# Kernel tuning notes

Measured on AMD Instinct MI355X. Metric: run time of the kernel, lower is better.

Reference implementation:

```python
import jax, jax.numpy as jnp
import numpy as np

B, S, T = 64, 49, 32
ENC, HID, EMB, VOCAB = 512, 512, 512, 32000
ATT = HID  # attention_dim = hidden_size in __init__


def setup_inputs() -> dict:
    key = jax.random.key(0)
    ks = jax.random.split(key, 20)
    def lin(k, out_d, in_d):
        s = 1.0 / np.sqrt(in_d)
        kw, kb = jax.random.split(k)
        return (jax.random.uniform(kw, (out_d, in_d), jnp.float32, -s, s),
                jax.random.uniform(kb, (out_d,), jnp.float32, -s, s))
    W_ih, b_ih = lin(ks[0], 3 * HID, EMB + ENC)
    W_hh, b_hh = lin(ks[1], 3 * HID, HID)
    W_out, b_out = lin(ks[2], VOCAB, HID)
    W_init, b_init = lin(ks[3], HID, ENC)
    W_beta, b_beta = lin(ks[4], ENC, HID)
    W_ea, b_ea = lin(ks[5], ATT, ENC)
    W_da, b_da = lin(ks[6], ATT, HID)
    W_fa, b_fa = lin(ks[7], 1, ATT)
    emb = jax.random.normal(ks[8], (VOCAB, EMB), jnp.float32)
    feats = jax.random.normal(ks[9], (B, S, ENC), jnp.float32)
    seq = jax.random.randint(ks[10], (B, T), 0, VOCAB)
    length = jax.random.randint(ks[11], (B,), 1, T + 1).at[0].set(T)
    return dict(feats=feats, seq=seq, length=length, emb=emb,
                W_ih=W_ih, b_ih=b_ih, W_hh=W_hh, b_hh=b_hh,
                W_out=W_out, b_out=b_out, W_init=W_init, b_init=b_init,
                W_beta=W_beta, b_beta=b_beta, W_ea=W_ea, b_ea=b_ea,
                W_da=W_da, b_da=b_da, W_fa=W_fa, b_fa=b_fa)


def _forward(feats, seq, length, emb, W_ih, b_ih, W_hh, b_hh, W_out, b_out,
             W_init, b_init, W_beta, b_beta, W_ea, b_ea, W_da, b_da, W_fa, b_fa):
    Tlen = seq.shape[1]
    embed_seq = emb[seq]                      # [B, T, EMB]
    embed_seq = jnp.swapaxes(embed_seq, 0, 1)  # [T, B, EMB]
    # active[t, b] = (length[b] > t); equivalent to torch's sorted shrinking batch
    active = (jnp.arange(Tlen)[:, None] < length[None, :])  # [T, B] bool
    h0 = jnp.mean(feats, axis=1) @ W_init.T + b_init         # [B, HID]
    scope0 = jnp.ones(feats.shape[:2], feats.dtype)          # [B, S]
    att1 = feats @ W_ea.T + b_ea                              # [B, S, ATT], hoisted

    def gru_cell(x, h):
        gi = x @ W_ih.T + b_ih
        gh = h @ W_hh.T + b_hh
        ir, iz, inn = jnp.split(gi, 3, axis=1)
        hr, hz, hn = jnp.split(gh, 3, axis=1)
        r = jax.nn.sigmoid(ir + hr)
        z = jax.nn.sigmoid(iz + hz)
        n = jnp.tanh(inn + r * hn)
        return (1.0 - z) * n + z * h

    def step(carry, xs):
        h, scope = carry
        embed_t, act = xs                     # [B, EMB], [B] bool
        actf = act[:, None].astype(h.dtype)
        att2 = h @ W_da.T + b_da              # [B, ATT]
        att = (jax.nn.relu(att1 + att2[:, None, :]) @ W_fa.T).squeeze(-1) + b_fa  # [B, S]
        alpha = jax.nn.softmax(att, axis=1)
        alpha_tilde = scope * alpha
        scope = jnp.where(act[:, None], scope * (1.0 - alpha), scope)
        awe = jnp.einsum('bse,bs->be', feats, alpha)          # [B, ENC]
        gate = jax.nn.sigmoid(h @ W_beta.T + b_beta)
        x = jnp.concatenate([embed_t, gate * awe], axis=1)
        h_new = gru_cell(x, h)
        h = jnp.where(act[:, None], h_new, h)
        preds = h_new @ W_out.T + b_out
        out_t = preds * actf
        alpha_out = alpha_tilde * actf
        return (h, scope), (out_t, alpha_out)

    (_, _), (output, alphas) = jax.lax.scan(step, (h0, scope0), (embed_seq, active))
    output = jnp.swapaxes(output, 0, 1)   # [B, T, VOCAB]
    alphas = jnp.swapaxes(alphas, 0, 1)   # [B, T, S]
    return output, alphas


def reference(feats, seq, length, emb, W_ih, b_ih, W_hh, b_hh, W_out, b_out,
              W_init, b_init, W_beta, b_beta, W_ea, b_ea, W_da, b_da, W_fa, b_fa):
    return _forward(feats, seq, length, emb, W_ih, b_ih, W_hh, b_hh, W_out, b_out,
                    W_init, b_init, W_beta, b_beta, W_ea, b_ea, W_da, b_da, W_fa, b_fa)
```

## Files before the change

### kernel.cpp

```cpp
#include <hip/hip_runtime.h>
#include <cstdint>
#include <cstddef>

#define B_   64
#define S_   49
#define T_   32
#define D_   512
#define V_   32000
#define G3   1536
#define NBLK 64

typedef float v4f   __attribute__((ext_vector_type(4)));
typedef int   i32x4 __attribute__((ext_vector_type(4)));
typedef _Float16 f16;
typedef _Float16 f16x8 __attribute__((ext_vector_type(8)));
typedef _Float16 f16x4 __attribute__((ext_vector_type(4)));

__device__ __forceinline__ float sigm(float x) { return 1.f / (1.f + __expf(-x)); }

__device__ __forceinline__ uint64_t ld_a64(const void* p) {
  return __hip_atomic_load((const uint64_t*)p, __ATOMIC_RELAXED, __HIP_MEMORY_SCOPE_AGENT);
}
__device__ __forceinline__ void st_a64(void* p, uint64_t v) {
  __hip_atomic_store((uint64_t*)p, v, __ATOMIC_RELAXED, __HIP_MEMORY_SCOPE_AGENT);
}
__device__ __forceinline__ uint32_t ld_a32(const void* p) {
  return __hip_atomic_load((const uint32_t*)p, __ATOMIC_RELAXED, __HIP_MEMORY_SCOPE_AGENT);
}
__device__ __forceinline__ void st_a32(void* p, uint32_t v) {
  __hip_atomic_store((uint32_t*)p, v, __ATOMIC_RELAXED, __HIP_MEMORY_SCOPE_AGENT);
}

__global__ __launch_bounds__(256) void k_cvt16(const float* __restrict__ in,
                                               f16* __restrict__ out) {
  int i = (blockIdx.x * 256 + threadIdx.x) * 8;
  float4 a = *(const float4*)(in + i);
  float4 b = *(const float4*)(in + i + 4);
  f16x8 o;
  o[0] = (f16)a.x; o[1] = (f16)a.y; o[2] = (f16)a.z; o[3] = (f16)a.w;
  o[4] = (f16)b.x; o[5] = (f16)b.y; o[6] = (f16)b.z; o[7] = (f16)b.w;
  *(f16x8*)(out + i) = o;
}

__global__ __launch_bounds__(128) void k_embed(const float* __restrict__ emb,
    const int* __restrict__ seq, const int* __restrict__ length,
    f16* __restrict__ xemb16, float* __restrict__ actmask) {
  int m = blockIdx.x;
  int t = m >> 6, b = m & 63;
  int idx = seq[b * T_ + t];
  float4 v = ((const float4*)(emb + (size_t)idx * D_))[threadIdx.x];
  f16x4 o;
  o[0] = (f16)v.x; o[1] = (f16)v.y; o[2] = (f16)v.z; o[3] = (f16)v.w;
  *(f16x4*)(xemb16 + (size_t)m * D_ + threadIdx.x * 4) = o;
  if (threadIdx.x == 0) actmask[b * T_ + t] = (t < length[b]) ? 1.f : 0.f;
}

__global__ __launch_bounds__(256) void k_hmean(const float* __restrict__ feats,
    float* __restrict__ hmean) {
  int b = blockIdx.x, tid = threadIdx.x;
  for (int e = tid; e < D_; e += 256) {
    float s = 0.f;
    for (int si = 0; si < S_; ++si) s += feats[((size_t)b * S_ + si) * D_ + e];
    hmean[b * D_ + e] = s * (1.f / 49.f);
  }
}

__global__ __launch_bounds__(256) void k_gemm_f32(
    float* __restrict__ C, const float* __restrict__ X, const float* __restrict__ W,
    const float* __restrict__ bias, int N, int K, int ldw) {
  __shared__ __align__(16) float XsT[32][68];
  __shared__ __align__(16) float WsT[32][68];
  const int nbase = blockIdx.x * 64, mbase = blockIdx.y * 64;
  const int tid = threadIdx.x;
  const int lr = tid >> 2;
  const int lk = (tid & 3) * 8;
  const int ty = tid >> 4, tx = tid & 15;
  float acc[4][4] = {};
  for (int k0 = 0; k0 < K; k0 += 32) {
    {
      const float* xs = X + (size_t)(mbase + lr) * K + k0 + lk;
      const float* wsrc = W + (size_t)(nbase + lr) * ldw + k0 + lk;
      float4 x0 = *(const float4*)xs, x1 = *(const float4*)(xs + 4);
      float4 w0 = *(const float4*)wsrc, w1 = *(const float4*)(wsrc + 4);
      XsT[lk + 0][lr] = x0.x; XsT[lk + 1][lr] = x0.y; XsT[lk + 2][lr] = x0.z; XsT[lk + 3][lr] = x0.w;
      XsT[lk + 4][lr] = x1.x; XsT[lk + 5][lr] = x1.y; XsT[lk + 6][lr] = x1.z; XsT[lk + 7][lr] = x1.w;
      WsT[lk + 0][lr] = w0.x; WsT[lk + 1][lr] = w0.y; WsT[lk + 2][lr] = w0.z; WsT[lk + 3][lr] = w0.w;
      WsT[lk + 4][lr] = w1.x; WsT[lk + 5][lr] = w1.y; WsT[lk + 6][lr] = w1.z; WsT[lk + 7][lr] = w1.w;
    }
    __syncthreads();
    #pragma unroll
    for (int kk = 0; kk < 32; ++kk) {
      float4 a4 = *(const float4*)&XsT[kk][ty * 4];
      float4 w4 = *(const float4*)&WsT[kk][tx * 4];
      float av[4] = {a4.x, a4.y, a4.z, a4.w};
      float wv[4] = {w4.x, w4.y, w4.z, w4.w};
      #pragma unroll
      for (int i = 0; i < 4; ++i)
        #pragma unroll
        for (int j = 0; j < 4; ++j)
          acc[i][j] = fmaf(av[i], wv[j], acc[i][j]);
    }
    __syncthreads();
  }
  #pragma unroll
  for (int i = 0; i < 4; ++i) {
    int m = mbase + ty * 4 + i;
    int n = nbase + tx * 4;
    float4 o;
    o.x = acc[i][0] + bias[n + 0];
    o.y = acc[i][1] + bias[n + 1];
    o.z = acc[i][2] + bias[n + 2];
    o.w = acc[i][3] + bias[n + 3];
    *(float4*)&C[(size_t)m * N + n] = o;
  }
}

#define GEMM16_CORE                                                            \
  __shared__ __align__(16) f16 As[128 * 32];                                   \
  __shared__ __align__(16) f16 Bs[128 * 32];                                   \
  const int tid = threadIdx.x;                                                 \
  const int l = tid & 63, w = tid >> 6;                                        \
  const int wr = w >> 1, wc = w & 1;                                           \
  const int lm = l & 15;                                                       \
  const int kc = l >> 4;                                                       \
  const int rchunk = (kc ^ ((lm >> 1) & 3)) * 8;                               \
  v4f acc[4][4];                                                               \
  _Pragma("unroll")                                                            \
  for (int mi = 0; mi < 4; ++mi)                                               \
    _Pragma("unroll")                                                          \
    for (int ni = 0; ni < 4; ++ni)                                             \
      acc[mi][ni] = (v4f){0.f, 0.f, 0.f, 0.f};                                 \
  i32x4 ra[2], rb[2];                                                          \
  auto LD = [&](int k0) {                                                      \
    _Pragma("unroll")                                                          \
    for (int i = 0; i < 2; ++i) {                                              \
      int ch = i * 256 + tid;                                                  \
      int row = ch >> 2, cq = ch & 3;                                          \
      ra[i] = *(const i32x4*)&A[(size_t)(mb + row) * 512 + k0 + cq * 8];       \
      rb[i] = *(const i32x4*)&Bw[(size_t)(nb + row) * 512 + k0 + cq * 8];      \
    }                                                                          \
  };                                                                           \
  LD(0);                                                                       \
  for (int k0 = 0; k0 < 512; k0 += 32) {                                       \
    _Pragma("unroll")                                                          \
    for (int i = 0; i < 2; ++i) {                                              \
      int ch = i * 256 + tid;                                                  \
      int row = ch >> 2, cq = ch & 3;                                          \
      int sc = (cq ^ ((row >> 1) & 3)) * 8;                                    \
      *(i32x4*)&As[row * 32 + sc] = ra[i];                                     \
      *(i32x4*)&Bs[row * 32 + sc] = rb[i];                                     \
    }                                                                          \
    __syncthreads();                                                           \
    if (k0 < 480) LD(k0 + 32);                                                 \
    f16x8 af[4], bf[4];                                                        \
    _Pragma("unroll")                                                          \
    for (int mi = 0; mi < 4; ++mi)                                             \
      af[mi] = *(const f16x8*)&As[(wr * 64 + mi * 16 + lm) * 32 + rchunk];     \
    _Pragma("unroll")                                                          \
    for (int ni = 0; ni < 4; ++ni)                                             \
      bf[ni] = *(const f16x8*)&Bs[(wc * 64 + ni * 16 + lm) * 32 + rchunk];     \
    _Pragma("unroll")                                                          \
    for (int mi = 0; mi < 4; ++mi)                                             \
      _Pragma("unroll")                                                        \
      for (int ni = 0; ni < 4; ++ni)                                           \
        acc[mi][ni] = __builtin_amdgcn_mfma_f32_16x16x32_f16(af[mi], bf[ni], acc[mi][ni], 0, 0, 0); \
    __syncthreads();                                                           \
  }

__global__ __launch_bounds__(256) void k_gemm16f(
    const f16* __restrict__ A, const f16* __restrict__ Bw,
    const float* __restrict__ bias, f16* __restrict__ out) {
  const int nb = blockIdx.x * 128, mb = blockIdx.y * 128;
  GEMM16_CORE
  #pragma unroll
  for (int ni = 0; ni < 4; ++ni) {
    int n = nb + wc * 64 + ni * 16 + lm;
    float bo = bias[n];
    #pragma unroll
    for (int mi = 0; mi < 4; ++mi) {
      int m0 = mb + wr * 64 + mi * 16 + (l >> 4) * 4;
      #pragma unroll
      for (int r = 0; r < 4; ++r) {
        int m = m0 + r;
        if (m < B_ * S_) out[(size_t)m * 512 + n] = (f16)(acc[mi][ni][r] + bo);
      }
    }
  }
}

__global__ __launch_bounds__(256) void k_gemm16g(
    const f16* __restrict__ A, const f16* __restrict__ Bw,
    const float* __restrict__ bias, float* __restrict__ out) {
  const int nb = blockIdx.x * 128, mb = blockIdx.y * 128;
  GEMM16_CORE
  #pragma unroll
  for (int ni = 0; ni < 4; ++ni) {
    int n = nb + wc * 64 + ni * 16 + lm;
    float bo = bias[n];
    int gate = n >> 9, rem = n & 511;
    int Kb = rem >> 3, jl = rem & 7;
    #pragma unroll
    for (int mi = 0; mi < 4; ++mi) {
      int m0 = mb + wr * 64 + mi * 16 + (l >> 4) * 4;
      int t = m0 >> 6, b0q = m0 & 63;
      float* dst = out + (((size_t)t * 64 + Kb) * 32 + gate * 8 + jl) * 64 + b0q;
      #pragma unroll
      for (int r = 0; r < 4; ++r)
        dst[r] = acc[mi][ni][r] + bo;
    }
  }
}

__global__ __launch_bounds__(256) void k_packW(
    const float* __restrict__ Wda, const float* __restrict__ Wbe,
    const float* __restrict__ Whh, const float* __restrict__ Wih,
    f16* __restrict__ Wp1, f16* __restrict__ Wp2, f16* __restrict__ Wp3) {
  int K = blockIdx.x, tid = threadIdx.x;
  for (int idx = tid; idx < 40 * 512; idx += 256) {
    int r = idx >> 9, e = idx & 511;
    float v;
    if (r < 8)       v = Wda[(size_t)(8 * K + r) * D_ + e];
    else if (r < 16) v = Wbe[(size_t)(8 * K + r - 8) * D_ + e];
    else if (r < 24) v = Whh[(size_t)(8 * K + r - 16) * D_ + e];
    else if (r < 32) v = Whh[(size_t)(512 + 8 * K + r - 24) * D_ + e];
    else             v = Whh[(size_t)(1024 + 8 * K + r - 32) * D_ + e];
    Wp1[(size_t)K * 20480 + idx] = (f16)v;
  }
  for (int idx = tid; idx < 24 * 512; idx += 256) {
    int r = idx >> 9, e = idx & 511;
    int g = r >> 3, jj = r & 7;
    float v = Wih[(size_t)(g * 512 + 8 * K + jj) * 1024 + 512 + e];
    Wp2[(size_t)K * 12288 + idx] = (f16)v;
  }
  for (int idx = tid; idx < 24 * 512; idx += 256) {
    int rl = idx >> 9, e = idx & 511;
    int r = K * 24 + rl;
    Wp3[(size_t)r * 512 + e] = (f16)Wih[(size_t)r * 1024 + e];
  }
}

__global__ __launch_bounds__(256) void k_packF(
    const float* __restrict__ feats, const float* __restrict__ h0,
    f16* __restrict__ feats16, f16* __restrict__ h16) {
  const int NF = B_ * S_ * D_;
  for (size_t i = blockIdx.x * 256 + threadIdx.x; i < NF + B_ * D_;
       i += (size_t)gridDim.x * 256) {
    if (i < NF) feats16[i] = (f16)feats[i];
    else        h16[i - NF] = (f16)h0[i - NF];
  }
}

__device__ __forceinline__ void wait_flags64(const int* __restrict__ flags,
                                             int target, int tid) {
  if (tid < 64) {
    while (!__all((int)ld_a32(flags + tid * 16) >= target)) {}
  }
  __syncthreads();
}

__device__ __forceinline__ void set_flag(int* slot, int val, int tid) {
  __syncthreads();
  if (tid == 0) st_a32(slot, (uint32_t)val);
}

__device__ __forceinline__ void stage_fast(const f16* __restrict__ src,
                                           uint4* __restrict__ hs, int tid) {
  const i32x4* s = (const i32x4*)src;
  i32x4 v[16];
  #pragma unroll
  for (int i = 0; i < 16; ++i) {
    asm volatile("global_load_dwordx4 %0, %1, off sc0 sc1"
                 : "=v"(v[i]) : "v"(s + i * 256 + tid));
  }
  asm volatile("s_waitcnt vmcnt(0)" ::: "memory");
  __builtin_amdgcn_sched_barrier(0);
  #pragma unroll
  for (int i = 0; i < 16; ++i) {
    int g = i * 256 + tid;
    int b = g >> 6, c = g & 63;
    *(i32x4*)&hs[b * 64 + (c ^ (b & 7))] = v[i];
  }
}

__global__ __launch_bounds__(256, 1) void k_recur(
    const f16* __restrict__ Wp1, const f16* __restrict__ Wp2,
    const f16* __restrict__ att116, const f16* __restrict__ feats16,
    const float* __restrict__ gi_pack,
    const float* __restrict__ b_da, const float* __restrict__ b_beta,
    const float* __restrict__ b_hh,
    const float* __restrict__ W_fa, const float* __restrict__ b_fa,
    const int* __restrict__ length,
    f16* __restrict__ h16, f16* __restrict__ xg16,
    float* __restrict__ att2g,
    float* __restrict__ alphas, f16* __restrict__ Hbuf,
    int* __restrict__ flags) {
  __shared__ __align__(16) uint4 lds_all[8704];
  __shared__ float gh_lds[24 * 72];
  __shared__ float gix_lds[24 * 72];
  __shared__ float att2_s[512];
  __shared__ float gate_s[512];
  __shared__ float att_s[64];
  __shared__ float alpha_s[64];
  uint4* hs = lds_all;
  uint4* W1 = lds_all + 4096;
  uint4* W2 = lds_all + 6656;
  float* attp = (float*)(lds_all + 8192);

  const int K = blockIdx.x, tid = threadIdx.x;
  const int w = tid >> 6, l = tid & 63;
  const int lm = l & 15, c4 = l >> 4;
  const int bq = tid & 63, jg = tid >> 6;
  const int jj0 = 2 * jg, jj1 = 2 * jg + 1;
  int* flagA = flags;
  int* flagB = flags + 1024;
  int* flagC = flags + 2048;

  {
    const uint4* s1 = (const uint4*)(Wp1 + (size_t)K * 20480);
    const uint4* s2 = (const uint4*)(Wp2 + (size_t)K * 12288);
    #pragma unroll
    for (int i = 0; i < 10; ++i) {
      int g = i * 256 + tid;
      int s = g >> 6, c = g & 63;
      W1[s * 64 + (c ^ (s & 7))] = s1[g];
    }
    #pragma unroll
    for (int i = 0; i < 6; ++i) {
      int g = i * 256 + tid;
      int s = g >> 6, c = g & 63;
      W2[s * 64 + (c ^ (s & 7))] = s2[g];
    }
  }
  const int lenB = length[K];
  const float bfa0 = b_fa[0];
  const int lb = length[bq];
  const float bhr0 = b_hh[8 * K + jj0],        bhr1 = b_hh[8 * K + jj1];
  const float bhz0 = b_hh[512 + 8 * K + jj0],  bhz1 = b_hh[512 + 8 * K + jj1];
  const float bhn0 = b_hh[1024 + 8 * K + jj0], bhn1 = b_hh[1024 + 8 * K + jj1];
  float wfa[8];
  {
    int a0i = l * 8;
    #pragma unroll
    for (int jx = 0; jx < 8; ++jx) wfa[jx] = W_fa[a0i + jx];
  }
  const float bda0 = b_da[2 * tid], bda1 = b_da[2 * tid + 1];
  const float bbe0 = b_beta[2 * tid], bbe1 = b_beta[2 * tid + 1];
  float scope_r = 1.f;
  __syncthreads();

  for (int t = 0; t < T_; ++t) {
    if (t) wait_flags64(flagC, t, tid);
    stage_fast(h16, hs, tid);
    __syncthreads();
    float hold0, hold1;
    {
      f16x8 hv = __builtin_bit_cast(f16x8, hs[bq * 64 + (K ^ (bq & 7))]);
      hold0 = (float)hv[jj0]; hold1 = (float)hv[jj1];
    }
    {
      v4f a0 = {0.f, 0.f, 0.f, 0.f};
      int bb = w * 16 + lm;
      #pragma unroll
      for (int kt = 0; kt < 16; ++kt) {
        int ca = kt * 4 + c4;
        f16x8 av = __builtin_bit_cast(f16x8, hs[bb * 64 + (ca ^ (bb & 7))]);
        f16x8 b0 = __builtin_bit_cast(f16x8, W1[lm * 64 + (ca ^ (lm & 7))]);
        a0 = __builtin_amdgcn_mfma_f32_16x16x32_f16(av, b0, a0, 0, 0, 0);
      }
      #pragma unroll
      for (int r = 0; r < 4; ++r)
        attp[(w * 16 + c4 * 4 + r) * 16 + lm] = a0[r];
    }
    __syncthreads();
    #pragma unroll
    for (int q = 0; q < 2; ++q) {
      int pp = tid * 2 + q;
      int bat = pp >> 3, pi = pp & 7;
      float2 f2;
      f2.x = attp[bat * 16 + 2 * pi];
      f2.y = attp[bat * 16 + 2 * pi + 1];
      size_t idx = (size_t)bat * 512 +
                   ((pi < 4) ? (4 * K + pi) : (256 + 4 * K + (pi - 4)));
      st_a64((uint64_t*)att2g + idx, __builtin_bit_cast(uint64_t, f2));
    }
    set_flag(flagA + K * 16, t + 1, tid);
    i32x4 attv[13];
    #pragma unroll
    for (int i = 0; i < 13; ++i) {
      int s = w + 4 * i;
      if (s < S_)
        attv[i] = *(const i32x4*)(att116 + ((size_t)K * S_ + s) * D_ + l * 8);
    }
    {
      v4f a1 = {0.f, 0.f, 0.f, 0.f};
      int bb = w * 16 + lm;
      #pragma unroll
      for (int kt = 0; kt < 16; ++kt) {
        int ca = kt * 4 + c4;
        f16x8 av = __builtin_bit_cast(f16x8, hs[bb * 64 + (ca ^ (bb & 7))]);
        f16x8 b1 = __builtin_bit_cast(f16x8, W1[(16 + lm) * 64 + (ca ^ ((16 + lm) & 7))]);
        a1 = __builtin_amdgcn_mfma_f32_16x16x32_f16(av, b1, a1, 0, 0, 0);
      }
      #pragma unroll
      for (int r = 0; r < 4; ++r)
        gh_lds[lm * 72 + (w * 16 + c4 * 4 + r)] = a1[r];
    }
    wait_flags64(flagA, t + 1, tid);
    {
      bool act = t < lenB;
      const uint64_t* arow2 = (const uint64_t*)att2g + (size_t)K * 512;
      {
        float2 f = __builtin_bit_cast(float2, ld_a64(arow2 + tid));
        att2_s[2 * tid]     = f.x + bda0;
        att2_s[2 * tid + 1] = f.y + bda1;
        float2 g = __builtin_bit_cast(float2, ld_a64(arow2 + tid + 256));
        gate_s[2 * tid]     = sigm(g.x + bbe0);
        gate_s[2 * tid + 1] = sigm(g.y + bbe1);
      }
      __syncthreads();
      int a0i = l * 8;
      #pragma unroll
      for (int i = 0; i < 13; ++i) {
        int s = w + 4 * i;
        if (s < S_) {
          f16x8 av = __builtin_bit_cast(f16x8, attv[i]);
          float p = 0.f;
          #pragma unroll
          for (int jx = 0; jx < 8; ++jx) {
            float v = (float)av[jx] + att2_s[a0i + jx];
            v = v > 0.f ? v : 0.f;
            p = fmaf(v, wfa[jx], p);
          }
          #pragma unroll
          for (int off = 32; off > 0; off >>= 1) p += __shfl_xor(p, off, 64);
          if (l == 0) att_s[s] = p + bfa0;
        }
      }
      __syncthreads();
      if (tid < 64) {
        float x = (tid < S_) ? att_s[tid] : -1e30f;
        float m = x;
        #pragma unroll
        for (int off = 32; off > 0; off >>= 1) m = fmaxf(m, __shfl_xor(m, off, 64));
        float e = (tid < S_) ? __expf(x - m) : 0.f;
        float su = e;
        #pragma unroll
        for (int off = 32; off > 0; off >>= 1) su += __shfl_xor(su, off, 64);
        if (tid < S_) alpha_s[tid] = e / su;
      }
      __syncthreads();
      if (tid < S_) {
        float al = alpha_s[tid];
        alphas[((size_t)K * T_ + t) * S_ + tid] = act ? scope_r * al : 0.f;
        scope_r = act ? scope_r * (1.f - al) : scope_r;
      }
      if (tid < 128) {
        int e0 = tid * 4;
        float s0 = 0.f, s1 = 0.f, s2 = 0.f, s3 = 0.f;
        #pragma unroll 7
        for (int s = 0; s < S_; ++s) {
          float al = alpha_s[s];
          f16x4 fv = *(const f16x4*)(feats16 + ((size_t)K * S_ + s) * D_ + e0);
          s0 = fmaf(al, (float)fv[0], s0);
          s1 = fmaf(al, (float)fv[1], s1);
          s2 = fmaf(al, (float)fv[2], s2);
          s3 = fmaf(al, (float)fv[3], s3);
        }
        f16x4 o;
        o[0] = (f16)(gate_s[e0 + 0] * s0);
        o[1] = (f16)(gate_s[e0 + 1] * s1);
        o[2] = (f16)(gate_s[e0 + 2] * s2);
        o[3] = (f16)(gate_s[e0 + 3] * s3);
        st_a64((uint64_t*)xg16 + (size_t)K * 128 + tid,
               __builtin_bit_cast(uint64_t, o));
      }
    }
    set_flag(flagB + K * 16, t + 1, tid);
    {
      v4f a2 = {0.f, 0.f, 0.f, 0.f};
      int bb = w * 16 + lm;
      #pragma unroll
      for (int kt = 0; kt < 16; ++kt) {
        int ca = kt * 4 + c4;
        f16x8 av = __builtin_bit_cast(f16x8, hs[bb * 64 + (ca ^ (bb & 7))]);
        f16x8 b2 = __builtin_bit_cast(f16x8, W1[(32 + lm) * 64 + (ca ^ ((32 + lm) & 7))]);
        a2 = __builtin_amdgcn_mfma_f32_16x16x32_f16(av, b2, a2, 0, 0, 0);
      }
      #pragma unroll
      for (int r = 0; r < 4; ++r)
        if (lm < 8) gh_lds[(16 + lm) * 72 + (w * 16 + c4 * 4 + r)] = a2[r];
    }
    wait_flags64(flagB, t + 1, tid);
    stage_fast(xg16, hs, tid);
    __syncthreads();
    {
      v4f c0 = {0.f,0.f,0.f,0.f}, c1 = {0.f,0.f,0.f,0.f};
      int bb = w * 16 + lm;
      #pragma unroll
      for (int kt = 0; kt < 16; ++kt) {
        int ca = kt * 4 + c4;
        f16x8 av = __builtin_bit_cast(f16x8, hs[bb * 64 + (ca ^ (bb & 7))]);
        f16x8 b0 = __builtin_bit_cast(f16x8, W2[lm * 64 + (ca ^ (lm & 7))]);
        f16x8 b1 = __builtin_bit_cast(f16x8, W2[(16 + lm) * 64 + (ca ^ ((16 + lm) & 7))]);
        c0 = __builtin_amdgcn_mfma_f32_16x16x32_f16(av, b0, c0, 0, 0, 0);
        c1 = __builtin_amdgcn_mfma_f32_16x16x32_f16(av, b1, c1, 0, 0, 0);
      }
      #pragma unroll
      for (int r = 0; r < 4; ++r) {
        int bat = w * 16 + c4 * 4 + r;
        gix_lds[lm * 72 + bat] = c0[r];
        if (lm < 8) gix_lds[(16 + lm) * 72 + bat] = c1[r];
      }
    }
    __syncthreads();
    {
      const float* gp = gi_pack + (size_t)(t * 64 + K) * 2048;
      float r0 = sigm(gix_lds[jj0 * 72 + bq] + gp[jj0 * 64 + bq] + gh_lds[jj0 * 72 + bq] + bhr0);
      float r1 = sigm(gix_lds[jj1 * 72 + bq] + gp[jj1 * 64 + bq] + gh_lds[jj1 * 72 + bq] + bhr1);
      float z0 = sigm(gix_lds[(8 + jj0) * 72 + bq] + gp[(8 + jj0) * 64 + bq] + gh_lds[(8 + jj0) * 72 + bq] + bhz0);
      float z1 = sigm(gix_lds[(8 + jj1) * 72 + bq] + gp[(8 + jj1) * 64 + bq] + gh_lds[(8 + jj1) * 72 + bq] + bhz1);
      float n0 = tanhf(gix_lds[(16 + jj0) * 72 + bq] + gp[(16 + jj0) * 64 + bq] + r0 * (gh_lds[(16 + jj0) * 72 + bq] + bhn0));
      float n1 = tanhf(gix_lds[(16 + jj1) * 72 + bq] + gp[(16 + jj1) * 64 + bq] + r1 * (gh_lds[(16 + jj1) * 72 + bq] + bhn1));
      float hn0 = (1.f - z0) * n0 + z0 * hold0;
      float hn1 = (1.f - z1) * n1 + z1 * hold1;
      bool act = t < lb;
      unsigned short u0 = __builtin_bit_cast(unsigned short, (f16)(act ? hn0 : hold0));
      unsigned short u1 = __builtin_bit_cast(unsigned short, (f16)(act ? hn1 : hold1));
      st_a32((uint32_t*)h16 + bq * 256 + 4 * K + jg,
             (uint32_t)u0 | ((uint32_t)u1 << 16));
      unsigned short p0 = __builtin_bit_cast(unsigned short, (f16)hn0);
      unsigned short p1 = __builtin_bit_cast(unsigned short, (f16)hn1);
      ((uint32_t*)Hbuf)[((size_t)bq * T_ + t) * 256 + 4 * K + jg] =
          (uint32_t)p0 | ((uint32_t)p1 << 16);
    }
    set_flag(flagC + K * 16, t + 1, tid);
  }
}

__global__ __launch_bounds__(256) void k_outgemm(
    const f16* __restrict__ A, const f16* __restrict__ Bw,
    const float* __restrict__ b_out, const float* __restrict__ actmask,
    float* __restrict__ out) {
  const int bid = blockIdx.x;
  const int swz = (bid & 7) * 500 + (bid >> 3);
  const int mb = (swz & 15) * 128;
  const int nb = (swz >> 4) * 128;
  GEMM16_CORE
  #pragma unroll
  for (int ni = 0; ni < 4; ++ni) {
    int n = nb + wc * 64 + ni * 16 + lm;
    float bo = b_out[n];
    #pragma unroll
    for (int mi = 0; mi < 4; ++mi) {
      int m0 = mb + wr * 64 + mi * 16 + (l >> 4) * 4;
      #pragma unroll
      for (int r = 0; r < 4; ++r) {
        int m = m0 + r;
        out[(size_t)m * V_ + n] = actmask[m] * (acc[mi][ni][r] + bo);
      }
    }
  }
}

extern "C" void kernel_launch(void* const* d_in, const int* in_sizes, int n_in,
                              void* d_out, int out_size, void* d_ws, size_t ws_size,
                              hipStream_t stream) {
  const float* feats  = (const float*)d_in[0];
  const int*   seq    = (const int*)d_in[1];
  const int*   length = (const int*)d_in[2];
  const float* emb    = (const float*)d_in[3];
  const float* W_ih   = (const float*)d_in[4];
  const float* b_ih   = (const float*)d_in[5];
  const float* W_hh   = (const float*)d_in[6];
  const float* b_hh   = (const float*)d_in[7];
  const float* W_out  = (const float*)d_in[8];
  const float* b_out  = (const float*)d_in[9];
  const float* W_init = (const float*)d_in[10];
  const float* b_init = (const float*)d_in[11];
  const float* W_beta = (const float*)d_in[12];
  const float* b_beta = (const float*)d_in[13];
  const float* W_ea   = (const float*)d_in[14];
  const float* b_ea   = (const float*)d_in[15];
  const float* W_da   = (const float*)d_in[16];
  const float* b_da   = (const float*)d_in[17];
  const float* W_fa   = (const float*)d_in[18];
  const float* b_fa   = (const float*)d_in[19];

  float* out    = (float*)d_out;
  float* alphas = out + (size_t)B_ * T_ * V_;

  float* ws = (float*)d_ws;
  int*   flags    = (int*)ws;        ws += 4096;
  float* h0       = ws;              ws += B_ * D_;
  float* hmean    = ws;              ws += B_ * D_;
  float* actmask  = ws;              ws += B_ * T_;
  float* att2g    = ws;              ws += B_ * 1024;
  float* gi_pack  = ws;              ws += (size_t)T_ * 64 * 32 * 64;
  f16* fp = (f16*)ws;
  f16* Woutb   = fp;  fp += (size_t)V_ * D_;
  f16* Hbuf    = fp;  fp += (size_t)B_ * T_ * D_;
  f16* Wp1     = fp;  fp += (size_t)64 * 20480;
  f16* Wp2     = fp;  fp += (size_t)64 * 12288;
  f16* Wp3     = fp;  fp += (size_t)G3 * D_;
  f16* Wea16   = fp;  fp += (size_t)D_ * D_;
  f16* xemb16  = fp;  fp += (size_t)B_ * T_ * D_;
  f16* feats16 = fp;  fp += (size_t)3200 * D_;
  f16* att116  = fp;  fp += (size_t)B_ * S_ * D_;
  f16* h16     = fp;  fp += B_ * D_;
  f16* xg16    = fp;  fp += B_ * D_;

  hipMemsetAsync(flags, 0, 16384, stream);

  k_cvt16<<<(V_ * D_) / 2048, 256, 0, stream>>>(W_out, Woutb);
  k_cvt16<<<(D_ * D_) / 2048, 256, 0, stream>>>(W_ea, Wea16);
  k_embed<<<B_ * T_, 128, 0, stream>>>(emb, seq, length, xemb16, actmask);
  k_hmean<<<B_, 256, 0, stream>>>(feats, hmean);
  k_gemm_f32<<<dim3(8, 1), 256, 0, stream>>>(h0, hmean, W_init, b_init, 512, 512, 512);
  k_packF<<<2048, 256, 0, stream>>>(feats, h0, feats16, h16);
  k_gemm16f<<<dim3(4, 25), 256, 0, stream>>>(feats16, Wea16, b_ea, att116);
  k_packW<<<64, 256, 0, stream>>>(W_da, W_beta, W_hh, W_ih, Wp1, Wp2, Wp3);
  k_gemm16g<<<dim3(12, 16), 256, 0, stream>>>(xemb16, Wp3, b_ih, gi_pack);

  k_recur<<<NBLK, 256, 0, stream>>>(Wp1, Wp2, att116, feats16, gi_pack,
      b_da, b_beta, b_hh, W_fa, b_fa, length,
      h16, xg16, att2g, alphas, Hbuf, flags);

  k_outgemm<<<4000, 256, 0, stream>>>(Hbuf, Woutb, b_out, actmask, out);
}
```

Before: 922.9 us.

## Fuse output projection into recurrent kernel via extra consumer blocks

Launches 192 extra blocks alongside the 64 recurrent blocks. The extra blocks convert W_out to fp16 and then, at each timestep, wait on the recurrence flags, load that step's hidden states and compute that step's slice of the vocabulary projection. The aim is to hide the large output GEMM and the weight conversion behind the latency-bound sequential recurrence, and to drop the separate cvt and outgemm launches. In exchange, the consumer blocks reread W_out from global or L2 every step with no LDS reuse, and they compete with the recurrent blocks for memory bandwidth. Correctness depends on all 256 blocks being co-resident.

Result: slower. 1.034 ms (+12.0%).

```diff
diff --git a/kernel.cpp b/kernel.cpp
--- a/kernel.cpp
+++ b/kernel.cpp
@@ -8,7 +8,7 @@
 #define D_   512
 #define V_   32000
 #define G3   1536
-#define NBLK 64
+#define NBLK 256
 
 typedef float v4f   __attribute__((ext_vector_type(4)));
 typedef int   i32x4 __attribute__((ext_vector_type(4)));
@@ -43,8 +43,7 @@
 }
 
 __global__ __launch_bounds__(128) void k_embed(const float* __restrict__ emb,
-    const int* __restrict__ seq, const int* __restrict__ length,
-    f16* __restrict__ xemb16, float* __restrict__ actmask) {
+    const int* __restrict__ seq, f16* __restrict__ xemb16) {
   int m = blockIdx.x;
   int t = m >> 6, b = m & 63;
   int idx = seq[b * T_ + t];
@@ -52,7 +51,6 @@
   f16x4 o;
   o[0] = (f16)v.x; o[1] = (f16)v.y; o[2] = (f16)v.z; o[3] = (f16)v.w;
   *(f16x4*)(xemb16 + (size_t)m * D_ + threadIdx.x * 4) = o;
-  if (threadIdx.x == 0) actmask[b * T_ + t] = (t < length[b]) ? 1.f : 0.f;
 }
 
 __global__ __launch_bounds__(256) void k_hmean(const float* __restrict__ feats,
@@ -293,6 +291,8 @@
     f16* __restrict__ h16, f16* __restrict__ xg16,
     float* __restrict__ att2g,
     float* __restrict__ alphas, f16* __restrict__ Hbuf,
+    const float* __restrict__ Wout, f16* __restrict__ Woutb,
+    const float* __restrict__ b_out, float* __restrict__ out,
     int* __restrict__ flags) {
   __shared__ __align__(16) uint4 lds_all[8704];
   __shared__ float gh_lds[24 * 72];
@@ -309,255 +309,321 @@
   const int K = blockIdx.x, tid = threadIdx.x;
   const int w = tid >> 6, l = tid & 63;
   const int lm = l & 15, c4 = l >> 4;
-  const int bq = tid & 63, jg = tid >> 6;
-  const int jj0 = 2 * jg, jj1 = 2 * jg + 1;
   int* flagA = flags;
   int* flagB = flags + 1024;
   int* flagC = flags + 2048;
 
-  {
-    const uint4* s1 = (const uint4*)(Wp1 + (size_t)K * 20480);
-    const uint4* s2 = (const uint4*)(Wp2 + (size_t)K * 12288);
-    #pragma unroll
-    for (int i = 0; i < 10; ++i) {
-      int g = i * 256 + tid;
-      int s = g >> 6, c = g & 63;
-      W1[s * 64 + (c ^ (s & 7))] = s1[g];
-    }
-    #pragma unroll
-    for (int i = 0; i < 6; ++i) {
-      int g = i * 256 + tid;
-      int s = g >> 6, c = g & 63;
-      W2[s * 64 + (c ^ (s & 7))] = s2[g];
-    }
-  }
-  const int lenB = length[K];
-  const float bfa0 = b_fa[0];
-  const int lb = length[bq];
-  const float bhr0 = b_hh[8 * K + jj0],        bhr1 = b_hh[8 * K + jj1];
-  const float bhz0 = b_hh[512 + 8 * K + jj0],  bhz1 = b_hh[512 + 8 * K + jj1];
-  const float bhn0 = b_hh[1024 + 8 * K + jj0], bhn1 = b_hh[1024 + 8 * K + jj1];
-  float wfa[8];
-  {
-    int a0i = l * 8;
-    #pragma unroll
-    for (int jx = 0; jx < 8; ++jx) wfa[jx] = W_fa[a0i + jx];
-  }
-  const float bda0 = b_da[2 * tid], bda1 = b_da[2 * tid + 1];
-  const float bbe0 = b_beta[2 * tid], bbe1 = b_beta[2 * tid + 1];
-  float scope_r = 1.f;
-  __syncthreads();
-
-  for (int t = 0; t < T_; ++t) {
-    if (t) wait_flags64(flagC, t, tid);
-    stage_fast(h16, hs, tid);
+  if (K < 64) {
+    const int bq = tid & 63, jg = tid >> 6;
+    const int jj0 = 2 * jg, jj1 = 2 * jg + 1;
+    {
+      const uint4* s1 = (const uint4*)(Wp1 + (size_t)K * 20480);
+      const uint4* s2 = (const uint4*)(Wp2 + (size_t)K * 12288);
+      #pragma unroll
+      for (int i = 0; i < 10; ++i) {
+        int g = i * 256 + tid;
+        int s = g >> 6, c = g & 63;
+        W1[s * 64 + (c ^ (s & 7))] = s1[g];
+      }
+      #pragma unroll
+      for (int i = 0; i < 6; ++i) {
+        int g = i * 256 + tid;
+        int s = g >> 6, c = g & 63;
+        W2[s * 64 + (c ^ (s & 7))] = s2[g];
+      }
+    }
+    const int lenB = length[K];
+    const float bfa0 = b_fa[0];
+    const int lb = length[bq];
+    const float bhr0 = b_hh[8 * K + jj0],        bhr1 = b_hh[8 * K + jj1];
+    const float bhz0 = b_hh[512 + 8 * K + jj0],  bhz1 = b_hh[512 + 8 * K + jj1];
+    const float bhn0 = b_hh[1024 + 8 * K + jj0], bhn1 = b_hh[1024 + 8 * K + jj1];
+    float wfa[8];
+    {
+      int a0i = l * 8;
+      #pragma unroll
+      for (int jx = 0; jx < 8; ++jx) wfa[jx] = W_fa[a0i + jx];
+    }
+    const float bda0 = b_da[2 * tid], bda1 = b_da[2 * tid + 1];
+    const float bbe0 = b_beta[2 * tid], bbe1 = b_beta[2 * tid + 1];
+    float scope_r = 1.f;
     __syncthreads();
-    float hold0, hold1;
-    {
-      f16x8 hv = __builtin_bit_cast(f16x8, hs[bq * 64 + (K ^ (bq & 7))]);
-      hold0 = (float)hv[jj0]; hold1 = (float)hv[jj1];
-    }
-    {
-      v4f a0 = {0.f, 0.f, 0.f, 0.f};
-      int bb = w * 16 + lm;
-      #pragma unroll
-      for (int kt = 0; kt < 16; ++kt) {
-        int ca = kt * 4 + c4;
-        f16x8 av = __builtin_bit_cast(f16x8, hs[bb * 64 + (ca ^ (bb & 7))]);
-        f16x8 b0 = __builtin_bit_cast(f16x8, W1[lm * 64 + (ca ^ (lm & 7))]);
-        a0 = __builtin_amdgcn_mfma_f32_16x16x32_f16(av, b0, a0, 0, 0, 0);
-      }
-      #pragma unroll
-      for (int r = 0; r < 4; ++r)
-        attp[(w * 16 + c4 * 4 + r) * 16 + lm] = a0[r];
-    }
-    __syncthreads();
-    #pragma unroll
-    for (int q = 0; q < 2; ++q) {
-      int pp = tid * 2 + q;
-      int bat = pp >> 3, pi = pp & 7;
-      float2 f2;
-      f2.x = attp[bat * 16 + 2 * pi];
-      f2.y = attp[bat * 16 + 2 * pi + 1];
-      size_t idx = (size_t)bat * 512 +
-                   ((pi < 4) ? (4 * K + pi) : (256 + 4 * K + (pi - 4)));
-      st_a64((uint64_t*)att2g + idx, __builtin_bit_cast(uint64_t, f2));
-    }
-    set_flag(flagA + K * 16, t + 1, tid);
-    i32x4 attv[13];
-    #pragma unroll
-    for (int i = 0; i < 13; ++i) {
-      int s = w + 4 * i;
-      if (s < S_)
-        attv[i] = *(const i32x4*)(att116 + ((size_t)K * S_ + s) * D_ + l * 8);
-    }
-    {
-      v4f a1 = {0.f, 0.f, 0.f, 0.f};
-      int bb = w * 16 + lm;
-      #pragma unroll
-      for (int kt = 0; kt < 16; ++kt) {
-        int ca = kt * 4 + c4;
-        f16x8 av = __builtin_bit_cast(f16x8, hs[bb * 64 + (ca ^ (bb & 7))]);
-        f16x8 b1 = __builtin_bit_cast(f16x8, W1[(16 + lm) * 64 + (ca ^ ((16 + lm) & 7))]);
-        a1 = __builtin_amdgcn_mfma_f32_16x16x32_f16(av, b1, a1, 0, 0, 0);
-      }
-      #pragma unroll
-      for (int r = 0; r < 4; ++r)
-        gh_lds[lm * 72 + (w * 16 + c4 * 4 + r)] = a1[r];
-    }
-    wait_flags64(flagA, t + 1, tid);
-    {
-      bool act = t < lenB;
-      const uint64_t* arow2 = (const uint64_t*)att2g + (size_t)K * 512;
-      {
-        float2 f = __builtin_bit_cast(float2, ld_a64(arow2 + tid));
-        att2_s[2 * tid]     = f.x + bda0;
-        att2_s[2 * tid + 1] = f.y + bda1;
-        float2 g = __builtin_bit_cast(float2, ld_a64(arow2 + tid + 256));
-        gate_s[2 * tid]     = sigm(g.x + bbe0);
-        gate_s[2 * tid + 1] = sigm(g.y + bbe1);
-      }
+
+    for (int t = 0; t < T_; ++t) {
+      if (t) wait_flags64(flagC, t, tid);
+      stage_fast(h16, hs, tid);
       __syncthreads();
-      int a0i = l * 8;
+      float hold0, hold1;
+      {
+        f16x8 hv = __builtin_bit_cast(f16x8, hs[bq * 64 + (K ^ (bq & 7))]);
+        hold0 = (float)hv[jj0]; hold1 = (float)hv[jj1];
+      }
+      {
+        v4f a0 = {0.f, 0.f, 0.f, 0.f};
+        int bb = w * 16 + lm;
+        #pragma unroll
+        for (int kt = 0; kt < 16; ++kt) {
+          int ca = kt * 4 + c4;
+          f16x8 av = __builtin_bit_cast(f16x8, hs[bb * 64 + (ca ^ (bb & 7))]);
+          f16x8 b0 = __builtin_bit_cast(f16x8, W1[lm * 64 + (ca ^ (lm & 7))]);
+          a0 = __builtin_amdgcn_mfma_f32_16x16x32_f16(av, b0, a0, 0, 0, 0);
+        }
+        #pragma unroll
+        for (int r = 0; r < 4; ++r)
+          attp[(w * 16 + c4 * 4 + r) * 16 + lm] = a0[r];
+      }
+      __syncthreads();
+      #pragma unroll
+      for (int q = 0; q < 2; ++q) {
+        int pp = tid * 2 + q;
+        int bat = pp >> 3, pi = pp & 7;
+        float2 f2;
+        f2.x = attp[bat * 16 + 2 * pi];
+        f2.y = attp[bat * 16 + 2 * pi + 1];
+        size_t idx = (size_t)bat * 512 +
+                     ((pi < 4) ? (4 * K + pi) : (256 + 4 * K + (pi - 4)));
+        st_a64((uint64_t*)att2g + idx, __builtin_bit_cast(uint64_t, f2));
+      }
+      set_flag(flagA + K * 16, t + 1, tid);
+      i32x4 attv[13];
       #pragma unroll
       for (int i = 0; i < 13; ++i) {
         int s = w + 4 * i;
-        if (s < S_) {
-          f16x8 av = __builtin_bit_cast(f16x8, attv[i]);
-          float p = 0.f;
+        if (s < S_)
+          attv[i] = *(const i32x4*)(att116 + ((size_t)K * S_ + s) * D_ + l * 8);
+      }
+      {
+        v4f a1 = {0.f, 0.f, 0.f, 0.f};
+        int bb = w * 16 + lm;
+        #pragma unroll
+        for (int kt = 0; kt < 16; ++kt) {
+          int ca = kt * 4 + c4;
+          f16x8 av = __builtin_bit_cast(f16x8, hs[bb * 64 + (ca ^ (bb & 7))]);
+          f16x8 b1 = __builtin_bit_cast(f16x8, W1[(16 + lm) * 64 + (ca ^ ((16 + lm) & 7))]);
+          a1 = __builtin_amdgcn_mfma_f32_16x16x32_f16(av, b1, a1, 0, 0, 0);
+        }
+        #pragma unroll
+        for (int r = 0; r < 4; ++r)
+          gh_lds[lm * 72 + (w * 16 + c4 * 4 + r)] = a1[r];
+      }
+      wait_flags64(flagA, t + 1, tid);
+      {
+        bool act = t < lenB;
+        const uint64_t* arow2 = (const uint64_t*)att2g + (size_t)K * 512;
+        {
+          float2 f = __builtin_bit_cast(float2, ld_a64(arow2 + tid));
+          att2_s[2 * tid]     = f.x + bda0;
+          att2_s[2 * tid + 1] = f.y + bda1;
+          float2 g = __builtin_bit_cast(float2, ld_a64(arow2 + tid + 256));
+          gate_s[2 * tid]     = sigm(g.x + bbe0);
+          gate_s[2 * tid + 1] = sigm(g.y + bbe1);
+        }
+        __syncthreads();
+        int a0i = l * 8;
+        #pragma unroll
+        for (int i = 0; i < 13; ++i) {
+          int s = w + 4 * i;
+          if (s < S_) {
+            f16x8 av = __builtin_bit_cast(f16x8, attv[i]);
+            float p = 0.f;
+            #pragma unroll
+            for (int jx = 0; jx < 8; ++jx) {
+              float v = (float)av[jx] + att2_s[a0i + jx];
+              v = v > 0.f ? v : 0.f;
+              p = fmaf(v, wfa[jx], p);
+            }
+            #pragma unroll
+            for (int off = 32; off > 0; off >>= 1) p += __shfl_xor(p, off, 64);
+            if (l == 0) att_s[s] = p + bfa0;
+          }
+        }
+        __syncthreads();
+        if (tid < 64) {
+          float x = (tid < S_) ? att_s[tid] : -1e30f;
+          float m = x;
           #pragma unroll
-          for (int jx = 0; jx < 8; ++jx) {
-            float v = (float)av[jx] + att2_s[a0i + jx];
-            v = v > 0.f ? v : 0.f;
-            p = fmaf(v, wfa[jx], p);
+          for (int off = 32; off > 0; off >>= 1) m = fmaxf(m, __shfl_xor(m, off, 64));
+          float e = (tid < S_) ? __expf(x - m) : 0.f;
+          float su = e;
+          #pragma unroll
+          for (int off = 32; off > 0; off >>= 1) su += __shfl_xor(su, off, 64);
+          if (tid < S_) alpha_s[tid] = e / su;
+        }
+        __syncthreads();
+        if (tid < S_) {
+          float al = alpha_s[tid];
+          alphas[((size_t)K * T_ + t) * S_ + tid] = act ? scope_r * al : 0.f;
+          scope_r = act ? scope_r * (1.f - al) : scope_r;
+        }
+        if (tid < 128) {
+          int e0 = tid * 4;
+          float s0 = 0.f, s1 = 0.f, s2 = 0.f, s3 = 0.f;
+          #pragma unroll 7
+          for (int s = 0; s < S_; ++s) {
+            float al = alpha_s[s];
+            f16x4 fv = *(const f16x4*)(feats16 + ((size_t)K * S_ + s) * D_ + e0);
+            s0 = fmaf(al, (float)fv[0], s0);
+            s1 = fmaf(al, (float)fv[1], s1);
+            s2 = fmaf(al, (float)fv[2], s2);
+            s3 = fmaf(al, (float)fv[3], s3);
+          }
+          f16x4 o;
+          o[0] = (f16)(gate_s[e0 + 0] * s0);
+          o[1] = (f16)(gate_s[e0 + 1] * s1);
+          o[2] = (f16)(gate_s[e0 + 2] * s2);
+          o[3] = (f16)(gate_s[e0 + 3] * s3);
+          st_a64((uint64_t*)xg16 + (size_t)K * 128 + tid,
+                 __builtin_bit_cast(uint64_t, o));
+        }
+      }
+      set_flag(flagB + K * 16, t + 1, tid);
+      {
+        v4f a2 = {0.f, 0.f, 0.f, 0.f};
+        int bb = w * 16 + lm;
+        #pragma unroll
+        for (int kt = 0; kt < 16; ++kt) {
+          int ca = kt * 4 + c4;
+          f16x8 av = __builtin_bit_cast(f16x8, hs[bb * 64 + (ca ^ (bb & 7))]);
+          f16x8 b2 = __builtin_bit_cast(f16x8, W1[(32 + lm) * 64 + (ca ^ ((32 + lm) & 7))]);
+          a2 = __builtin_amdgcn_mfma_f32_16x16x32_f16(av, b2, a2, 0, 0, 0);
+        }
+        #pragma unroll
+        for (int r = 0; r < 4; ++r)
+          if (lm < 8) gh_lds[(16 + lm) * 72 + (w * 16 + c4 * 4 + r)] = a2[r];
+      }
+      wait_flags64(flagB, t + 1, tid);
+      stage_fast(xg16, hs, tid);
+      __syncthreads();
+      {
+        v4f c0 = {0.f,0.f,0.f,0.f}, c1 = {0.f,0.f,0.f,0.f};
+        int bb = w * 16 + lm;
+        #pragma unroll
+        for (int kt = 0; kt < 16; ++kt) {
+          int ca = kt * 4 + c4;
+          f16x8 av = __builtin_bit_cast(f16x8, hs[bb * 64 + (ca ^ (bb & 7))]);
+          f16x8 b0 = __builtin_bit_cast(f16x8, W2[lm * 64 + (ca ^ (lm & 7))]);
+          f16x8 b1 = __builtin_bit_cast(f16x8, W2[(16 + lm) * 64 + (ca ^ ((16 + lm) & 7))]);
+          c0 = __builtin_amdgcn_mfma_f32_16x16x32_f16(av, b0, c0, 0, 0, 0);
+          c1 = __builtin_amdgcn_mfma_f32_16x16x32_f16(av, b1, c1, 0, 0, 0);
+        }
+        #pragma unroll
+        for (int r = 0; r < 4; ++r) {
+          int bat = w * 16 + c4 * 4 + r;
+          gix_lds[lm * 72 + bat] = c0[r];
+          if (lm < 8) gix_lds[(16 + lm) * 72 + bat] = c1[r];
+        }
+      }
+      __syncthreads();
+      {
+        const float* gp = gi_pack + (size_t)(t * 64 + K) * 2048;
+        float r0 = sigm(gix_lds[jj0 * 72 + bq] + gp[jj0 * 64 + bq] + gh_lds[jj0 * 72 + bq] + bhr0);
+        float r1 = sigm(gix_lds[jj1 * 72 + bq] + gp[jj1 * 64 + bq] + gh_lds[jj1 * 72 + bq] + bhr1);
+        float z0 = sigm(gix_lds[(8 + jj0) * 72 + bq] + gp[(8 + jj0) * 64 + bq] + gh_lds[(8 + jj0) * 72 + bq] + bhz0);
+        float z1 = sigm(gix_lds[(8 + jj1) * 72 + bq] + gp[(8 + jj1) * 64 + bq] + gh_lds[(8 + jj1) * 72 + bq] + bhz1);
+        float n0 = tanhf(gix_lds[(16 + jj0) * 72 + bq] + gp[(16 + jj0) * 64 + bq] + r0 * (gh_lds[(16 + jj0) * 72 + bq] + bhn0));
+        float n1 = tanhf(gix_lds[(16 + jj1) * 72 + bq] + gp[(16 + jj1) * 64 + bq] + r1 * (gh_lds[(16 + jj1) * 72 + bq] + bhn1));
+        float hn0 = (1.f - z0) * n0 + z0 * hold0;
+        float hn1 = (1.f - z1) * n1 + z1 * hold1;
+        bool act = t < lb;
+        unsigned short u0 = __builtin_bit_cast(unsigned short, (f16)(act ? hn0 : hold0));
+        unsigned short u1 = __builtin_bit_cast(unsigned short, (f16)(act ? hn1 : hold1));
+        st_a32((uint32_t*)h16 + bq * 256 + 4 * K + jg,
+               (uint32_t)u0 | ((uint32_t)u1 << 16));
+        unsigned short p0 = __builtin_bit_cast(unsigned short, (f16)hn0);
+        unsigned short p1 = __builtin_bit_cast(unsigned short, (f16)hn1);
+        st_a32((uint32_t*)Hbuf + ((size_t)bq * T_ + t) * 256 + 4 * K + jg,
+               (uint32_t)p0 | ((uint32_t)p1 << 16));
+      }
+      set_flag(flagC + K * 16, t + 1, tid);
+    }
+  } else {
+    const int widx = K - 64;
+    for (int tile = widx; tile < 250; tile += 192) {
+      const float* src = Wout + (size_t)tile * 128 * 512;
+      f16* dst = Woutb + (size_t)tile * 128 * 512;
+      for (int i = tid; i < 128 * 128; i += 256) {
+        float4 v = ((const float4*)src)[i];
+        f16x4 o;
+        o[0] = (f16)v.x; o[1] = (f16)v.y; o[2] = (f16)v.z; o[3] = (f16)v.w;
+        *(f16x4*)(dst + i * 4) = o;
+      }
+    }
+    int lenw[4];
+    #pragma unroll
+    for (int mi = 0; mi < 4; ++mi) lenw[mi] = length[mi * 16 + c4 * 4];
+    int len4[4];
+    __syncthreads();
+
+    for (int t = 0; t < T_; ++t) {
+      if (tid < 64) {
+        while (!__all((int)ld_a32(flagC + tid * 16) >= t + 1))
+          __builtin_amdgcn_s_sleep(32);
+      }
+      __syncthreads();
+      {
+        i32x4 v[16];
+        #pragma unroll
+        for (int i = 0; i < 16; ++i) {
+          int g = i * 256 + tid;
+          int b = g >> 6, c = g & 63;
+          const i32x4* p = (const i32x4*)(Hbuf + (((size_t)b * T_ + t) << 9)) + c;
+          asm volatile("global_load_dwordx4 %0, %1, off sc0 sc1"
+                       : "=v"(v[i]) : "v"(p));
+        }
+        asm volatile("s_waitcnt vmcnt(0)" ::: "memory");
+        __builtin_amdgcn_sched_barrier(0);
+        #pragma unroll
+        for (int i = 0; i < 16; ++i) {
+          int g = i * 256 + tid;
+          int b = g >> 6, c = g & 63;
+          *(i32x4*)&hs[b * 64 + (c ^ (b & 7))] = v[i];
+        }
+      }
+      __syncthreads();
+      for (int tile = widx; tile < 250; tile += 192) {
+        int n0 = tile * 128 + w * 32;
+        v4f acc[4][2];
+        #pragma unroll
+        for (int mi = 0; mi < 4; ++mi) {
+          acc[mi][0] = (v4f){0.f, 0.f, 0.f, 0.f};
+          acc[mi][1] = (v4f){0.f, 0.f, 0.f, 0.f};
+        }
+        i32x4 bc[2], bn[2];
+        #pragma unroll
+        for (int nf = 0; nf < 2; ++nf)
+          bc[nf] = *(const i32x4*)&Woutb[(size_t)(n0 + nf * 16 + lm) * 512 + c4 * 8];
+        for (int kt = 0; kt < 16; ++kt) {
+          if (kt < 15) {
+            #pragma unroll
+            for (int nf = 0; nf < 2; ++nf)
+              bn[nf] = *(const i32x4*)&Woutb[(size_t)(n0 + nf * 16 + lm) * 512 + (kt + 1) * 32 + c4 * 8];
           }
           #pragma unroll
-          for (int off = 32; off > 0; off >>= 1) p += __shfl_xor(p, off, 64);
-          if (l == 0) att_s[s] = p + bfa0;
+          for (int mi = 0; mi < 4; ++mi) {
+            int row = mi * 16 + lm;
+            int ca = kt * 4 + c4;
+            f16x8 av = __builtin_bit_cast(f16x8, hs[row * 64 + (ca ^ (row & 7))]);
+            acc[mi][0] = __builtin_amdgcn_mfma_f32_16x16x32_f16(av, __builtin_bit_cast(f16x8, bc[0]), acc[mi][0], 0, 0, 0);
+            acc[mi][1] = __builtin_amdgcn_mfma_f32_16x16x32_f16(av, __builtin_bit_cast(f16x8, bc[1]), acc[mi][1], 0, 0, 0);
+          }
+          bc[0] = bn[0]; bc[1] = bn[1];
+        }
+        #pragma unroll
+        for (int nf = 0; nf < 2; ++nf) {
+          int n = n0 + nf * 16 + lm;
+          float bo = b_out[n];
+          #pragma unroll
+          for (int mi = 0; mi < 4; ++mi) {
+            #pragma unroll
+            for (int r = 0; r < 4; ++r) {
+              int b = mi * 16 + c4 * 4 + r;
+              float val = (t < length[b]) ? (acc[mi][nf][r] + bo) : 0.f;
+              out[((size_t)b * T_ + t) * V_ + n] = val;
+            }
+          }
         }
       }
       __syncthreads();
-      if (tid < 64) {
-        float x = (tid < S_) ? att_s[tid] : -1e30f;
-        float m = x;
-        #pragma unroll
-        for (int off = 32; off > 0; off >>= 1) m = fmaxf(m, __shfl_xor(m, off, 64));
-        float e = (tid < S_) ? __expf(x - m) : 0.f;
-        float su = e;
-        #pragma unroll
-        for (int off = 32; off > 0; off >>= 1) su += __shfl_xor(su, off, 64);
-        if (tid < S_) alpha_s[tid] = e / su;
-      }
-      __syncthreads();
-      if (tid < S_) {
-        float al = alpha_s[tid];
-        alphas[((size_t)K * T_ + t) * S_ + tid] = act ? scope_r * al : 0.f;
-        scope_r = act ? scope_r * (1.f - al) : scope_r;
-      }
-      if (tid < 128) {
-        int e0 = tid * 4;
-        float s0 = 0.f, s1 = 0.f, s2 = 0.f, s3 = 0.f;
-        #pragma unroll 7
-        for (int s = 0; s < S_; ++s) {
-          float al = alpha_s[s];
-          f16x4 fv = *(const f16x4*)(feats16 + ((size_t)K * S_ + s) * D_ + e0);
-          s0 = fmaf(al, (float)fv[0], s0);
-          s1 = fmaf(al, (float)fv[1], s1);
-          s2 = fmaf(al, (float)fv[2], s2);
-          s3 = fmaf(al, (float)fv[3], s3);
-        }
-        f16x4 o;
-        o[0] = (f16)(gate_s[e0 + 0] * s0);
-        o[1] = (f16)(gate_s[e0 + 1] * s1);
-        o[2] = (f16)(gate_s[e0 + 2] * s2);
-        o[3] = (f16)(gate_s[e0 + 3] * s3);
-        st_a64((uint64_t*)xg16 + (size_t)K * 128 + tid,
-               __builtin_bit_cast(uint64_t, o));
-      }
-    }
-    set_flag(flagB + K * 16, t + 1, tid);
-    {
-      v4f a2 = {0.f, 0.f, 0.f, 0.f};
-      int bb = w * 16 + lm;
-      #pragma unroll
-      for (int kt = 0; kt < 16; ++kt) {
-        int ca = kt * 4 + c4;
-        f16x8 av = __builtin_bit_cast(f16x8, hs[bb * 64 + (ca ^ (bb & 7))]);
-        f16x8 b2 = __builtin_bit_cast(f16x8, W1[(32 + lm) * 64 + (ca ^ ((32 + lm) & 7))]);
-        a2 = __builtin_amdgcn_mfma_f32_16x16x32_f16(av, b2, a2, 0, 0, 0);
-      }
-      #pragma unroll
-      for (int r = 0; r < 4; ++r)
-        if (lm < 8) gh_lds[(16 + lm) * 72 + (w * 16 + c4 * 4 + r)] = a2[r];
-    }
-    wait_flags64(flagB, t + 1, tid);
-    stage_fast(xg16, hs, tid);
-    __syncthreads();
-    {
-      v4f c0 = {0.f,0.f,0.f,0.f}, c1 = {0.f,0.f,0.f,0.f};
-      int bb = w * 16 + lm;
-      #pragma unroll
-      for (int kt = 0; kt < 16; ++kt) {
-        int ca = kt * 4 + c4;
-        f16x8 av = __builtin_bit_cast(f16x8, hs[bb * 64 + (ca ^ (bb & 7))]);
-        f16x8 b0 = __builtin_bit_cast(f16x8, W2[lm * 64 + (ca ^ (lm & 7))]);
-        f16x8 b1 = __builtin_bit_cast(f16x8, W2[(16 + lm) * 64 + (ca ^ ((16 + lm) & 7))]);
-        c0 = __builtin_amdgcn_mfma_f32_16x16x32_f16(av, b0, c0, 0, 0, 0);
-        c1 = __builtin_amdgcn_mfma_f32_16x16x32_f16(av, b1, c1, 0, 0, 0);
-      }
-      #pragma unroll
-      for (int r = 0; r < 4; ++r) {
-        int bat = w * 16 + c4 * 4 + r;
-        gix_lds[lm * 72 + bat] = c0[r];
-        if (lm < 8) gix_lds[(16 + lm) * 72 + bat] = c1[r];
-      }
-    }
-    __syncthreads();
-    {
-      const float* gp = gi_pack + (size_t)(t * 64 + K) * 2048;
-      float r0 = sigm(gix_lds[jj0 * 72 + bq] + gp[jj0 * 64 + bq] + gh_lds[jj0 * 72 + bq] + bhr0);
-      float r1 = sigm(gix_lds[jj1 * 72 + bq] + gp[jj1 * 64 + bq] + gh_lds[jj1 * 72 + bq] + bhr1);
-      float z0 = sigm(gix_lds[(8 + jj0) * 72 + bq] + gp[(8 + jj0) * 64 + bq] + gh_lds[(8 + jj0) * 72 + bq] + bhz0);
-      float z1 = sigm(gix_lds[(8 + jj1) * 72 + bq] + gp[(8 + jj1) * 64 + bq] + gh_lds[(8 + jj1) * 72 + bq] + bhz1);
-      float n0 = tanhf(gix_lds[(16 + jj0) * 72 + bq] + gp[(16 + jj0) * 64 + bq] + r0 * (gh_lds[(16 + jj0) * 72 + bq] + bhn0));
-      float n1 = tanhf(gix_lds[(16 + jj1) * 72 + bq] + gp[(16 + jj1) * 64 + bq] + r1 * (gh_lds[(16 + jj1) * 72 + bq] + bhn1));
-      float hn0 = (1.f - z0) * n0 + z0 * hold0;
-      float hn1 = (1.f - z1) * n1 + z1 * hold1;
-      bool act = t < lb;
-      unsigned short u0 = __builtin_bit_cast(unsigned short, (f16)(act ? hn0 : hold0));
-      unsigned short u1 = __builtin_bit_cast(unsigned short, (f16)(act ? hn1 : hold1));
-      st_a32((uint32_t*)h16 + bq * 256 + 4 * K + jg,
-             (uint32_t)u0 | ((uint32_t)u1 << 16));
-      unsigned short p0 = __builtin_bit_cast(unsigned short, (f16)hn0);
-      unsigned short p1 = __builtin_bit_cast(unsigned short, (f16)hn1);
-      ((uint32_t*)Hbuf)[((size_t)bq * T_ + t) * 256 + 4 * K + jg] =
-          (uint32_t)p0 | ((uint32_t)p1 << 16);
-    }
-    set_flag(flagC + K * 16, t + 1, tid);
-  }
-}
-
-__global__ __launch_bounds__(256) void k_outgemm(
-    const f16* __restrict__ A, const f16* __restrict__ Bw,
-    const float* __restrict__ b_out, const float* __restrict__ actmask,
-    float* __restrict__ out) {
-  const int bid = blockIdx.x;
-  const int swz = (bid & 7) * 500 + (bid >> 3);
-  const int mb = (swz & 15) * 128;
-  const int nb = (swz >> 4) * 128;
-  GEMM16_CORE
-  #pragma unroll
-  for (int ni = 0; ni < 4; ++ni) {
-    int n = nb + wc * 64 + ni * 16 + lm;
-    float bo = b_out[n];
-    #pragma unroll
-    for (int mi = 0; mi < 4; ++mi) {
-      int m0 = mb + wr * 64 + mi * 16 + (l >> 4) * 4;
-      #pragma unroll
-      for (int r = 0; r < 4; ++r) {
-        int m = m0 + r;
-        out[(size_t)m * V_ + n] = actmask[m] * (acc[mi][ni][r] + bo);
-      }
     }
   }
 }
@@ -593,7 +659,6 @@
   int*   flags    = (int*)ws;        ws += 4096;
   float* h0       = ws;              ws += B_ * D_;
   float* hmean    = ws;              ws += B_ * D_;
-  float* actmask  = ws;              ws += B_ * T_;
   float* att2g    = ws;              ws += B_ * 1024;
   float* gi_pack  = ws;              ws += (size_t)T_ * 64 * 32 * 64;
   f16* fp = (f16*)ws;
@@ -611,9 +676,8 @@
 
   hipMemsetAsync(flags, 0, 16384, stream);
 
-  k_cvt16<<<(V_ * D_) / 2048, 256, 0, stream>>>(W_out, Woutb);
   k_cvt16<<<(D_ * D_) / 2048, 256, 0, stream>>>(W_ea, Wea16);
-  k_embed<<<B_ * T_, 128, 0, stream>>>(emb, seq, length, xemb16, actmask);
+  k_embed<<<B_ * T_, 128, 0, stream>>>(emb, seq, xemb16);
   k_hmean<<<B_, 256, 0, stream>>>(feats, hmean);
   k_gemm_f32<<<dim3(8, 1), 256, 0, stream>>>(h0, hmean, W_init, b_init, 512, 512, 512);
   k_packF<<<2048, 256, 0, stream>>>(feats, h0, feats16, h16);
@@ -623,7 +687,6 @@
 
   k_recur<<<NBLK, 256, 0, stream>>>(Wp1, Wp2, att116, feats16, gi_pack,
       b_da, b_beta, b_hh, W_fa, b_fa, length,
-      h16, xg16, att2g, alphas, Hbuf, flags);
-
-  k_outgemm<<<4000, 256, 0, stream>>>(Hbuf, Woutb, b_out, actmask, out);
-}
+      h16, xg16, att2g, alphas, Hbuf,
+      W_out, Woutb, b_out, out, flags);
+}
```
